# Kernel optimization log

Measured on AMD Instinct MI355X. Metric: run time of the kernel, lower is better.

## Reference

```python
import jax, jax.numpy as jnp
import numpy as np
import math

N_EMBD = 64
HEAD_SIZE = 64
B, T = 16, 2048


def setup_inputs() -> dict:
    key = jax.random.key(0)
    k1, k2, k3, k4 = jax.random.split(key, 4)
    inputs = jax.random.normal(k1, (B, T, N_EMBD), dtype=jnp.float32)
    # Causal mask: True where attention is NOT allowed (upper triangle),
    # matching masked_fill_(mask, -1e9) with mask = ~tril.
    mask = jnp.triu(jnp.ones((T, T), dtype=bool), k=1)
    # nn.Linear(n_embd, head_size, bias=False) weights, stored as
    # (n_embd, head_size) so projection is inputs @ W (== x @ W_torch.T).
    scale = 1.0 / math.sqrt(N_EMBD)
    Wq = jax.random.uniform(k2, (N_EMBD, HEAD_SIZE), jnp.float32, -scale, scale)
    Wk = jax.random.uniform(k3, (N_EMBD, HEAD_SIZE), jnp.float32, -scale, scale)
    Wv = jax.random.uniform(k4, (N_EMBD, HEAD_SIZE), jnp.float32, -scale, scale)
    return {"inputs": inputs, "mask": mask, "Wq": Wq, "Wk": Wk, "Wv": Wv}


def reference(inputs, mask, Wq, Wk, Wv):
    # inputs: (B, T, n_embd); mask: (T, T) bool broadcast over batch
    q = inputs @ Wq  # (B, T, H)
    k = inputs @ Wk  # (B, T, H)
    v = inputs @ Wv  # (B, T, H)
    inv_sqrt_h = 1.0 / math.sqrt(HEAD_SIZE)
    scores = jnp.einsum('bth,bsh->bts', q, k) * inv_sqrt_h  # (B, T, T)
    scores = jnp.where(mask, jnp.float32(-1e9), scores)
    attention = jax.nn.softmax(scores, axis=-1)
    out = jnp.einsum('bts,bsh->bth', attention, v)  # (B, T, H)
    return out
```

## Files before the change

### kernel.cpp

```cpp
#include <hip/hip_runtime.h>
#include <stdint.h>


typedef __bf16 bf16x8 __attribute__((ext_vector_type(8)));
typedef __bf16 bf16x4 __attribute__((ext_vector_type(4)));
typedef float f32x4 __attribute__((ext_vector_type(4)));

#define QSCALE 0.18033688011112042f
#define MFMA16(a, b, c) __builtin_amdgcn_mfma_f32_16x16x32_bf16((a), (b), (c), 0, 0, 0)

__device__ __forceinline__ unsigned short f2bf(float f) {
  union { float f; unsigned u; } x; x.f = f;
  unsigned r = x.u + 0x7fffu + ((x.u >> 16) & 1u);
  return (unsigned short)(r >> 16);
}

__device__ __forceinline__ int swz(int row, int bytecol) {
  return row * 128 + (bytecol ^ ((row & 7) << 4));
}
__device__ __forceinline__ bf16x8 frag(const unsigned short* base, int row, int kf, int lane) {
  int off = swz(row, kf * 64 + ((lane >> 4) << 4));
  return *(const bf16x8*)((const char*)base + off);
}

__device__ __forceinline__ void gload_lds16(const unsigned short* g, unsigned short* l) {
  __builtin_amdgcn_global_load_lds(
      (const __attribute__((address_space(1))) unsigned int*)g,
      (__attribute__((address_space(3))) unsigned int*)l, 16, 0, 0);
}

__global__ __launch_bounds__(256, 2) void proj_kernel(
    const float* __restrict__ X, const float* __restrict__ Wq,
    const float* __restrict__ Wk, const float* __restrict__ Wv,
    unsigned short* __restrict__ Qg, unsigned short* __restrict__ Kg,
    unsigned short* __restrict__ Vtg) {
  __shared__ __align__(16) unsigned short Xs[64 * 64];
  __shared__ __align__(16) unsigned short Ws[3 * 64 * 64];
  const int tid = threadIdx.x, lane = tid & 63, w = tid >> 6;
  const int ln = lane & 15, g = lane >> 4;
  const long grow0 = (long)blockIdx.x * 64;
  const int b = (int)(grow0 >> 11);
  const int tin0 = (int)(grow0 & 2047);

  {
    const int r = tid >> 2, c = tid & 3;
    const float* src = X + (grow0 + r) * 64 + c * 16;
    float4 f0 = *(const float4*)src;
    float4 f1 = *(const float4*)(src + 4);
    float4 f2 = *(const float4*)(src + 8);
    float4 f3 = *(const float4*)(src + 12);
    uint4 d0, d1;
    d0.x = f2bf(f0.x) | ((unsigned)f2bf(f0.y) << 16);
    d0.y = f2bf(f0.z) | ((unsigned)f2bf(f0.w) << 16);
    d0.z = f2bf(f1.x) | ((unsigned)f2bf(f1.y) << 16);
    d0.w = f2bf(f1.z) | ((unsigned)f2bf(f1.w) << 16);
    d1.x = f2bf(f2.x) | ((unsigned)f2bf(f2.y) << 16);
    d1.y = f2bf(f2.z) | ((unsigned)f2bf(f2.w) << 16);
    d1.z = f2bf(f3.x) | ((unsigned)f2bf(f3.y) << 16);
    d1.w = f2bf(f3.z) | ((unsigned)f2bf(f3.w) << 16);
    *(uint4*)((char*)Xs + swz(r, c * 32)) = d0;
    *(uint4*)((char*)Xs + swz(r, c * 32 + 16)) = d1;
  }
  for (int c = tid; c < 3 * 4096; c += 256) {
    const int mat = c >> 12, rr = c & 4095;
    const int e = rr >> 6, hh = rr & 63;
    const float* wsrc = (mat == 0) ? Wq : (mat == 1) ? Wk : Wv;
    *(unsigned short*)((char*)(Ws + mat * 4096) + swz(hh, e * 2)) = f2bf(wsrc[rr]);
  }
  __syncthreads();

  const f32x4 zero = {0.f, 0.f, 0.f, 0.f};
#pragma unroll
  for (int i = 0; i < 3; ++i) {
    const int task = w * 3 + i;
    const int mat = task >> 2, s = task & 3;
    const unsigned short* wbase = Ws + mat * 4096;
    if (mat < 2) {
      bf16x8 a0 = frag(Xs, s * 16 + ln, 0, lane);
      bf16x8 a1 = frag(Xs, s * 16 + ln, 1, lane);
      unsigned short* dst = mat ? Kg : Qg;
#pragma unroll
      for (int nt = 0; nt < 4; ++nt) {
        bf16x8 b0 = frag(wbase, nt * 16 + ln, 0, lane);
        bf16x8 b1 = frag(wbase, nt * 16 + ln, 1, lane);
        f32x4 acc = MFMA16(a0, b0, zero);
        acc = MFMA16(a1, b1, acc);
        long row0 = grow0 + s * 16 + g * 4;
        int col = nt * 16 + ln;
#pragma unroll
        for (int k = 0; k < 4; ++k) {
          float v = acc[k];
          if (mat == 0) v *= QSCALE;
          dst[(row0 + k) * 64 + col] = f2bf(v);
        }
      }
    } else {
      bf16x8 a0 = frag(wbase, s * 16 + ln, 0, lane);
      bf16x8 a1 = frag(wbase, s * 16 + ln, 1, lane);
#pragma unroll
      for (int nt = 0; nt < 4; ++nt) {
        bf16x8 b0 = frag(Xs, nt * 16 + ln, 0, lane);
        bf16x8 b1 = frag(Xs, nt * 16 + ln, 1, lane);
        f32x4 acc = MFMA16(a0, b0, zero);
        acc = MFMA16(a1, b1, acc);
        int t = tin0 + nt * 16 + ln;
        int h0 = s * 16 + g * 4;
#pragma unroll
        for (int k = 0; k < 4; ++k)
          Vtg[((long)(b * 64 + h0 + k)) * 2048 + t] = f2bf(acc[k]);
      }
    }
  }
}

__global__ __launch_bounds__(256, 4) void attn8_kernel(
    const unsigned short* __restrict__ Qg, const unsigned short* __restrict__ Kg,
    const unsigned short* __restrict__ Vtg, float* __restrict__ Og) {
  __shared__ __align__(16) unsigned char smem[35840];

  const int bid = blockIdx.x;
  const int slot = bid >> 3;
  const int b = ((bid & 7) << 1) + (slot & 1);
  const int j = slot >> 1;
  const int qt = (j & 1) ? (j >> 1) : 63 - (j >> 1);
  const int q0 = qt * 32;
  const int ns = (q0 + 95) >> 6;

  const int tid = threadIdx.x;
  const int lane = tid & 63, w = tid >> 6;
  const int g = lane >> 4, ln = lane & 15;
  const int h = w & 1, qh = w >> 1;

  const unsigned short* qrow = Qg + ((long)b * 2048 + q0 + qh * 16 + ln) * 64;
  const bf16x8 qb0 = *(const bf16x8*)(qrow + g * 8);
  const bf16x8 qb1 = *(const bf16x8*)(qrow + 32 + g * 8);

  const unsigned short* kbase = Kg + (long)b * 2048 * 64;
  const unsigned short* vbase = Vtg + (long)b * 64 * 2048;

  const int sw32 = (w & 1) * 32;
  const int cxor = ((lane & 7) ^ ((lane >> 3) & 7)) * 8;
  const int klane = (lane >> 3) * 64 + cxor;
  const int vlane = (lane >> 3) * 2048 + cxor;

  const f32x4 zero = {0.f, 0.f, 0.f, 0.f};
  f32x4 o[4];
#pragma unroll
  for (int nt = 0; nt < 4; ++nt) o[nt] = zero;
  float den = 0.f;

  if (w < 2) {
#pragma unroll
    for (int i = 0; i < 4; ++i)
      gload_lds16(kbase + (long)(sw32 + i * 8) * 64 + klane,
                  (unsigned short*)smem + (sw32 + i * 8) * 64);
  } else {
#pragma unroll
    for (int i = 0; i < 4; ++i)
      gload_lds16(vbase + (long)(sw32 + i * 8) * 2048 + vlane,
                  (unsigned short*)(smem + 8192) + (sw32 + i * 8) * 64);
  }
  __syncthreads();

  int cur = 0;
  for (int t = 0; t < ns; ++t) {
    const int kv0 = t * 64;
    if (t + 1 < ns) {
      const int kvn = kv0 + 64;
      unsigned short* dstK = (unsigned short*)(smem + (cur ^ 1) * 16384);
      unsigned short* dstV = (unsigned short*)(smem + (cur ^ 1) * 16384 + 8192);
      if (w < 2) {
#pragma unroll
        for (int i = 0; i < 4; ++i)
          gload_lds16(kbase + (long)(kvn + sw32 + i * 8) * 64 + klane,
                      dstK + (sw32 + i * 8) * 64);
      } else {
#pragma unroll
        for (int i = 0; i < 4; ++i)
          gload_lds16(vbase + (long)(sw32 + i * 8) * 2048 + kvn + vlane,
                      dstV + (sw32 + i * 8) * 64);
      }
    }

    const unsigned short* Kb = (const unsigned short*)(smem + cur * 16384);
    const unsigned char*  Vb = smem + cur * 16384 + 8192;

    bf16x8 ka00 = frag(Kb, h * 32 + ln,      0, lane);
    bf16x8 ka01 = frag(Kb, h * 32 + ln,      1, lane);
    bf16x8 ka10 = frag(Kb, h * 32 + 16 + ln, 0, lane);
    bf16x8 ka11 = frag(Kb, h * 32 + 16 + ln, 1, lane);

    bf16x8 vb[4];
#pragma unroll
    for (int nt = 0; nt < 4; ++nt) {
      int row = nt * 16 + ln;
      bf16x4 lo = *(const bf16x4*)(Vb + swz(row, h * 64 + g * 8));
      bf16x4 hi = *(const bf16x4*)(Vb + swz(row, h * 64 + 32 + g * 8));
      vb[nt] = __builtin_shufflevector(lo, hi, 0, 1, 2, 3, 4, 5, 6, 7);
    }

    __builtin_amdgcn_s_setprio(1);
    f32x4 st0 = MFMA16(ka00, qb0, zero);  st0 = MFMA16(ka01, qb1, st0);
    f32x4 st1 = MFMA16(ka10, qb0, zero);  st1 = MFMA16(ka11, qb1, st1);
    __builtin_amdgcn_s_setprio(0);

    if (t == ns - 1) {
      const int qg = q0 + qh * 16 + ln;
      const int kvb = kv0 + h * 32 + g * 4;
#pragma unroll
      for (int i = 0; i < 4; ++i) {
        if (kvb + i > qg)      st0[i] = -1e30f;
        if (kvb + 16 + i > qg) st1[i] = -1e30f;
      }
    }

    bf16x8 pa;
#pragma unroll
    for (int i = 0; i < 4; ++i) {
      float p0 = exp2f(st0[i]);
      float p1 = exp2f(st1[i]);
      den += p0 + p1;
      pa[i] = (__bf16)p0;
      pa[4 + i] = (__bf16)p1;
    }

    __builtin_amdgcn_s_setprio(1);
#pragma unroll
    for (int nt = 0; nt < 4; ++nt)
      o[nt] = MFMA16(pa, vb[nt], o[nt]);
    __builtin_amdgcn_s_setprio(0);

    __syncthreads();
    cur ^= 1;
  }

  den += __shfl_xor(den, 16);
  den += __shfl_xor(den, 32);

  float* Olds = (float*)smem;
  float* Dlds = (float*)(smem + 34816);
#pragma unroll
  for (int nt = 0; nt < 4; ++nt)
#pragma unroll
    for (int i = 0; i < 4; ++i)
      Olds[(w * 16 + g * 4 + i) * 68 + nt * 16 + ln] = o[nt][i];
  if (lane < 16) Dlds[w * 16 + ln] = den;
  __syncthreads();

  const int q = tid >> 3;
  const int qhx = q >> 4, r = q & 15;
  const int d0 = (tid & 7) * 8;
  float dd = Dlds[(qhx * 2) * 16 + r] + Dlds[(qhx * 2 + 1) * 16 + r];
  float inv = 1.0f / dd;
  float acc[8];
#pragma unroll
  for (int e = 0; e < 8; ++e)
    acc[e] = (Olds[((qhx * 2) * 16 + r) * 68 + d0 + e] +
              Olds[((qhx * 2 + 1) * 16 + r) * 68 + d0 + e]) * inv;
  float* outp = Og + ((long)b * 2048 + q0 + q) * 64 + d0;
  *(float4*)outp = make_float4(acc[0], acc[1], acc[2], acc[3]);
  *(float4*)(outp + 4) = make_float4(acc[4], acc[5], acc[6], acc[7]);
}

extern "C" void kernel_launch(void* const* d_in, const int* in_sizes, int n_in,
                              void* d_out, int out_size, void* d_ws, size_t ws_size,
                              hipStream_t stream) {
  const float* X  = (const float*)d_in[0];
  const float* Wq = (const float*)d_in[2];
  const float* Wk = (const float*)d_in[3];
  const float* Wv = (const float*)d_in[4];

  unsigned short* Qg  = (unsigned short*)d_ws;
  unsigned short* Kg  = Qg + 2097152;
  unsigned short* Vtg = Kg + 2097152;

  proj_kernel<<<512, 256, 0, stream>>>(X, Wq, Wk, Wv, Qg, Kg, Vtg);
  attn8_kernel<<<1024, 256, 0, stream>>>(Qg, Kg, Vtg, (float*)d_out);
}
```

Measured before the change: 47.60 us.

## Triple-buffer K/V staging with one barrier per iteration

```diff
diff --git a/kernel.cpp b/kernel.cpp
--- a/kernel.cpp
+++ b/kernel.cpp
@@ -113,10 +113,10 @@
   }
 }
 
-__global__ __launch_bounds__(256, 4) void attn8_kernel(
+__global__ __launch_bounds__(256, 3) void attn9_kernel(
     const unsigned short* __restrict__ Qg, const unsigned short* __restrict__ Kg,
     const unsigned short* __restrict__ Vtg, float* __restrict__ Og) {
-  __shared__ __align__(16) unsigned char smem[35840];
+  __shared__ __align__(16) unsigned char smem[49152];
 
   const int bid = blockIdx.x;
   const int slot = bid >> 3;
@@ -142,6 +142,7 @@
   const int cxor = ((lane & 7) ^ ((lane >> 3) & 7)) * 8;
   const int klane = (lane >> 3) * 64 + cxor;
   const int vlane = (lane >> 3) * 2048 + cxor;
+  const bool stagesK = (w < 2);
 
   const f32x4 zero = {0.f, 0.f, 0.f, 0.f};
   f32x4 o[4];
@@ -149,41 +150,41 @@
   for (int nt = 0; nt < 4; ++nt) o[nt] = zero;
   float den = 0.f;
 
-  if (w < 2) {
-#pragma unroll
-    for (int i = 0; i < 4; ++i)
-      gload_lds16(kbase + (long)(sw32 + i * 8) * 64 + klane,
-                  (unsigned short*)smem + (sw32 + i * 8) * 64);
-  } else {
-#pragma unroll
-    for (int i = 0; i < 4; ++i)
-      gload_lds16(vbase + (long)(sw32 + i * 8) * 2048 + vlane,
-                  (unsigned short*)(smem + 8192) + (sw32 + i * 8) * 64);
-  }
-  __syncthreads();
+  auto stage = [&](int t, int bi) {
+    unsigned short* dstK = (unsigned short*)(smem + bi * 16384);
+    unsigned short* dstV = dstK + 4096;
+    const int kv0s = t * 64;
+    if (stagesK) {
+#pragma unroll
+      for (int i = 0; i < 4; ++i)
+        gload_lds16(kbase + (long)(kv0s + sw32 + i * 8) * 64 + klane,
+                    dstK + (sw32 + i * 8) * 64);
+    } else {
+#pragma unroll
+      for (int i = 0; i < 4; ++i)
+        gload_lds16(vbase + (long)(sw32 + i * 8) * 2048 + kv0s + vlane,
+                    dstV + (sw32 + i * 8) * 64);
+    }
+  };
+
+  stage(0, 0);
+  if (ns > 1) stage(1, 1);
 
   int cur = 0;
   for (int t = 0; t < ns; ++t) {
-    const int kv0 = t * 64;
-    if (t + 1 < ns) {
-      const int kvn = kv0 + 64;
-      unsigned short* dstK = (unsigned short*)(smem + (cur ^ 1) * 16384);
-      unsigned short* dstV = (unsigned short*)(smem + (cur ^ 1) * 16384 + 8192);
-      if (w < 2) {
-#pragma unroll
-        for (int i = 0; i < 4; ++i)
-          gload_lds16(kbase + (long)(kvn + sw32 + i * 8) * 64 + klane,
-                      dstK + (sw32 + i * 8) * 64);
-      } else {
-#pragma unroll
-        for (int i = 0; i < 4; ++i)
-          gload_lds16(vbase + (long)(sw32 + i * 8) * 2048 + kvn + vlane,
-                      dstV + (sw32 + i * 8) * 64);
-      }
+    if (t == ns - 1) asm volatile("s_waitcnt vmcnt(0)" ::: "memory");
+    else             asm volatile("s_waitcnt vmcnt(4)" ::: "memory");
+    __builtin_amdgcn_s_barrier();
+    __builtin_amdgcn_sched_barrier(0);
+
+    if (t + 2 < ns) {
+      int nxt = cur + 2; if (nxt >= 3) nxt -= 3;
+      stage(t + 2, nxt);
     }
 
     const unsigned short* Kb = (const unsigned short*)(smem + cur * 16384);
     const unsigned char*  Vb = smem + cur * 16384 + 8192;
+    const int kv0 = t * 64;
 
     bf16x8 ka00 = frag(Kb, h * 32 + ln,      0, lane);
     bf16x8 ka01 = frag(Kb, h * 32 + ln,      1, lane);
@@ -230,12 +231,13 @@
       o[nt] = MFMA16(pa, vb[nt], o[nt]);
     __builtin_amdgcn_s_setprio(0);
 
-    __syncthreads();
-    cur ^= 1;
+    ++cur; if (cur >= 3) cur -= 3;
   }
 
   den += __shfl_xor(den, 16);
   den += __shfl_xor(den, 32);
+
+  __syncthreads();
 
   float* Olds = (float*)smem;
   float* Dlds = (float*)(smem + 34816);
@@ -275,5 +277,5 @@
   unsigned short* Vtg = Kg + 2097152;
 
   proj_kernel<<<512, 256, 0, stream>>>(X, Wq, Wk, Wv, Qg, Kg, Vtg);
-  attn8_kernel<<<1024, 256, 0, stream>>>(Qg, Kg, Vtg, (float*)d_out);
-}
+  attn9_kernel<<<1024, 256, 0, stream>>>(Qg, Kg, Vtg, (float*)d_out);
+}
```

Result: slower. 53.67 us (+12.8%).

## Enlarge attention query tile to 64 with per-wave KV split and triple-buffered K

Applied to the files above, without the earlier changes.

```diff
diff --git a/kernel.cpp b/kernel.cpp
--- a/kernel.cpp
+++ b/kernel.cpp
@@ -113,153 +113,195 @@
   }
 }
 
-__global__ __launch_bounds__(256, 4) void attn8_kernel(
+__global__ __launch_bounds__(256, 2) void attn10_kernel(
     const unsigned short* __restrict__ Qg, const unsigned short* __restrict__ Kg,
     const unsigned short* __restrict__ Vtg, float* __restrict__ Og) {
-  __shared__ __align__(16) unsigned char smem[35840];
+  __shared__ __align__(16) unsigned char smem[49152];
 
   const int bid = blockIdx.x;
-  const int slot = bid >> 3;
-  const int b = ((bid & 7) << 1) + (slot & 1);
-  const int j = slot >> 1;
-  const int qt = (j & 1) ? (j >> 1) : 63 - (j >> 1);
-  const int q0 = qt * 32;
-  const int ns = (q0 + 95) >> 6;
+  const int xcd = bid & 7, idx = bid >> 3;
+  const int b = (xcd << 1) + (idx & 1);
+  const int m = idx >> 1;
+  const int qt = (idx & 1) ? (31 - m) : m;
+  const int q0 = qt * 64;
+  const int ns = (q0 + 191) >> 7;
 
   const int tid = threadIdx.x;
   const int lane = tid & 63, w = tid >> 6;
   const int g = lane >> 4, ln = lane & 15;
-  const int h = w & 1, qh = w >> 1;
-
-  const unsigned short* qrow = Qg + ((long)b * 2048 + q0 + qh * 16 + ln) * 64;
-  const bf16x8 qb0 = *(const bf16x8*)(qrow + g * 8);
-  const bf16x8 qb1 = *(const bf16x8*)(qrow + 32 + g * 8);
+
+  const unsigned short* qrow = Qg + ((long)b * 2048 + q0) * 64;
+  bf16x8 qb[4][2];
+#pragma unroll
+  for (int nq = 0; nq < 4; ++nq)
+#pragma unroll
+    for (int kf = 0; kf < 2; ++kf)
+      qb[nq][kf] = *(const bf16x8*)(qrow + (nq * 16 + ln) * 64 + kf * 32 + g * 8);
 
   const unsigned short* kbase = Kg + (long)b * 2048 * 64;
   const unsigned short* vbase = Vtg + (long)b * 64 * 2048;
 
-  const int sw32 = (w & 1) * 32;
-  const int cxor = ((lane & 7) ^ ((lane >> 3) & 7)) * 8;
-  const int klane = (lane >> 3) * 64 + cxor;
-  const int vlane = (lane >> 3) * 2048 + cxor;
+  const int klane = ((lane >> 3) << 6) + (((lane & 7) ^ ((lane >> 3) & 7)) << 3);
+  unsigned short* kslice = (unsigned short*)(smem + w * 4096);
 
   const f32x4 zero = {0.f, 0.f, 0.f, 0.f};
-  f32x4 o[4];
-#pragma unroll
-  for (int nt = 0; nt < 4; ++nt) o[nt] = zero;
-  float den = 0.f;
-
-  if (w < 2) {
+  f32x4 o[4][4];
+#pragma unroll
+  for (int nq = 0; nq < 4; ++nq)
+#pragma unroll
+    for (int nt = 0; nt < 4; ++nt) o[nq][nt] = zero;
+  float den[4] = {0.f, 0.f, 0.f, 0.f};
+
+  {
+    const unsigned short* kg0 = kbase + (long)(w * 32) * 64 + klane;
 #pragma unroll
     for (int i = 0; i < 4; ++i)
-      gload_lds16(kbase + (long)(sw32 + i * 8) * 64 + klane,
-                  (unsigned short*)smem + (sw32 + i * 8) * 64);
-  } else {
-#pragma unroll
-    for (int i = 0; i < 4; ++i)
-      gload_lds16(vbase + (long)(sw32 + i * 8) * 2048 + vlane,
-                  (unsigned short*)(smem + 8192) + (sw32 + i * 8) * 64);
-  }
-  __syncthreads();
+      gload_lds16(kg0 + i * 512, kslice + i * 512);
+    if (ns > 1) {
+      const unsigned short* kg1 = kbase + (long)(128 + w * 32) * 64 + klane;
+#pragma unroll
+      for (int i = 0; i < 4; ++i)
+        gload_lds16(kg1 + i * 512, (unsigned short*)((char*)kslice + 16384) + i * 512);
+    }
+  }
 
   int cur = 0;
   for (int t = 0; t < ns; ++t) {
-    const int kv0 = t * 64;
-    if (t + 1 < ns) {
-      const int kvn = kv0 + 64;
-      unsigned short* dstK = (unsigned short*)(smem + (cur ^ 1) * 16384);
-      unsigned short* dstV = (unsigned short*)(smem + (cur ^ 1) * 16384 + 8192);
-      if (w < 2) {
-#pragma unroll
-        for (int i = 0; i < 4; ++i)
-          gload_lds16(kbase + (long)(kvn + sw32 + i * 8) * 64 + klane,
-                      dstK + (sw32 + i * 8) * 64);
-      } else {
-#pragma unroll
-        for (int i = 0; i < 4; ++i)
-          gload_lds16(vbase + (long)(sw32 + i * 8) * 2048 + kvn + vlane,
-                      dstV + (sw32 + i * 8) * 64);
+    const int kv0w = t * 128 + w * 32;
+
+    const unsigned short* vr = vbase + (long)ln * 2048 + kv0w + g * 4;
+    bf16x4 vl0 = *(const bf16x4*)vr;
+    bf16x4 vh0 = *(const bf16x4*)(vr + 16);
+    bf16x4 vl1 = *(const bf16x4*)(vr + 16 * 2048);
+    bf16x4 vh1 = *(const bf16x4*)(vr + 16 * 2048 + 16);
+    bf16x4 vl2 = *(const bf16x4*)(vr + 32 * 2048);
+    bf16x4 vh2 = *(const bf16x4*)(vr + 32 * 2048 + 16);
+    bf16x4 vl3 = *(const bf16x4*)(vr + 48 * 2048);
+    bf16x4 vh3 = *(const bf16x4*)(vr + 48 * 2048 + 16);
+
+    if (t + 2 < ns) {
+      int nb = cur + 2; if (nb >= 3) nb -= 3;
+      const unsigned short* kg = kbase + (long)((t + 2) * 128 + w * 32) * 64 + klane;
+      unsigned short* dst = (unsigned short*)((char*)kslice + nb * 16384);
+#pragma unroll
+      for (int i = 0; i < 4; ++i)
+        gload_lds16(kg + i * 512, dst + i * 512);
+    }
+
+    if (t + 2 < ns)      asm volatile("s_waitcnt vmcnt(16)" ::: "memory");
+    else if (t + 1 < ns) asm volatile("s_waitcnt vmcnt(12)" ::: "memory");
+    else                 asm volatile("s_waitcnt vmcnt(8)"  ::: "memory");
+    __builtin_amdgcn_sched_barrier(0);
+
+    const unsigned short* Kb = (const unsigned short*)((char*)kslice + cur * 16384);
+
+    bf16x8 ka00 = frag(Kb, ln, 0, lane);
+    bf16x8 ka01 = frag(Kb, ln, 1, lane);
+    bf16x8 ka10 = frag(Kb, 16 + ln, 0, lane);
+    bf16x8 ka11 = frag(Kb, 16 + ln, 1, lane);
+
+    f32x4 st[2][4];
+    __builtin_amdgcn_s_setprio(1);
+#pragma unroll
+    for (int nq = 0; nq < 4; ++nq) {
+      f32x4 a = MFMA16(ka00, qb[nq][0], zero);
+      st[0][nq] = MFMA16(ka01, qb[nq][1], a);
+      f32x4 c = MFMA16(ka10, qb[nq][0], zero);
+      st[1][nq] = MFMA16(ka11, qb[nq][1], c);
+    }
+    __builtin_amdgcn_s_setprio(0);
+
+    if (t == ns - 1) {
+#pragma unroll
+      for (int s = 0; s < 2; ++s)
+#pragma unroll
+        for (int nq = 0; nq < 4; ++nq) {
+          const int qg = q0 + nq * 16 + ln;
+          const int kvb = kv0w + s * 16 + g * 4;
+#pragma unroll
+          for (int i = 0; i < 4; ++i)
+            if (kvb + i > qg) st[s][nq][i] = -1e30f;
+        }
+    }
+
+    bf16x8 pa[4];
+#pragma unroll
+    for (int nq = 0; nq < 4; ++nq)
+#pragma unroll
+      for (int i = 0; i < 4; ++i) {
+        float p0 = exp2f(st[0][nq][i]);
+        float p1 = exp2f(st[1][nq][i]);
+        den[nq] += p0 + p1;
+        pa[nq][i] = (__bf16)p0;
+        pa[nq][4 + i] = (__bf16)p1;
       }
-    }
-
-    const unsigned short* Kb = (const unsigned short*)(smem + cur * 16384);
-    const unsigned char*  Vb = smem + cur * 16384 + 8192;
-
-    bf16x8 ka00 = frag(Kb, h * 32 + ln,      0, lane);
-    bf16x8 ka01 = frag(Kb, h * 32 + ln,      1, lane);
-    bf16x8 ka10 = frag(Kb, h * 32 + 16 + ln, 0, lane);
-    bf16x8 ka11 = frag(Kb, h * 32 + 16 + ln, 1, lane);
-
-    bf16x8 vb[4];
-#pragma unroll
-    for (int nt = 0; nt < 4; ++nt) {
-      int row = nt * 16 + ln;
-      bf16x4 lo = *(const bf16x4*)(Vb + swz(row, h * 64 + g * 8));
-      bf16x4 hi = *(const bf16x4*)(Vb + swz(row, h * 64 + 32 + g * 8));
-      vb[nt] = __builtin_shufflevector(lo, hi, 0, 1, 2, 3, 4, 5, 6, 7);
-    }
 
     __builtin_amdgcn_s_setprio(1);
-    f32x4 st0 = MFMA16(ka00, qb0, zero);  st0 = MFMA16(ka01, qb1, st0);
-    f32x4 st1 = MFMA16(ka10, qb0, zero);  st1 = MFMA16(ka11, qb1, st1);
+    {
+      bf16x8 vb = __builtin_shufflevector(vl0, vh0, 0, 1, 2, 3, 4, 5, 6, 7);
+#pragma unroll
+      for (int nq = 0; nq < 4; ++nq) o[nq][0] = MFMA16(pa[nq], vb, o[nq][0]);
+      vb = __builtin_shufflevector(vl1, vh1, 0, 1, 2, 3, 4, 5, 6, 7);
+#pragma unroll
+      for (int nq = 0; nq < 4; ++nq) o[nq][1] = MFMA16(pa[nq], vb, o[nq][1]);
+      vb = __builtin_shufflevector(vl2, vh2, 0, 1, 2, 3, 4, 5, 6, 7);
+#pragma unroll
+      for (int nq = 0; nq < 4; ++nq) o[nq][2] = MFMA16(pa[nq], vb, o[nq][2]);
+      vb = __builtin_shufflevector(vl3, vh3, 0, 1, 2, 3, 4, 5, 6, 7);
+#pragma unroll
+      for (int nq = 0; nq < 4; ++nq) o[nq][3] = MFMA16(pa[nq], vb, o[nq][3]);
+    }
     __builtin_amdgcn_s_setprio(0);
 
-    if (t == ns - 1) {
-      const int qg = q0 + qh * 16 + ln;
-      const int kvb = kv0 + h * 32 + g * 4;
-#pragma unroll
-      for (int i = 0; i < 4; ++i) {
-        if (kvb + i > qg)      st0[i] = -1e30f;
-        if (kvb + 16 + i > qg) st1[i] = -1e30f;
-      }
-    }
-
-    bf16x8 pa;
-#pragma unroll
-    for (int i = 0; i < 4; ++i) {
-      float p0 = exp2f(st0[i]);
-      float p1 = exp2f(st1[i]);
-      den += p0 + p1;
-      pa[i] = (__bf16)p0;
-      pa[4 + i] = (__bf16)p1;
-    }
-
-    __builtin_amdgcn_s_setprio(1);
-#pragma unroll
-    for (int nt = 0; nt < 4; ++nt)
-      o[nt] = MFMA16(pa, vb[nt], o[nt]);
-    __builtin_amdgcn_s_setprio(0);
-
-    __syncthreads();
-    cur ^= 1;
-  }
-
-  den += __shfl_xor(den, 16);
-  den += __shfl_xor(den, 32);
-
+    ++cur; if (cur >= 3) cur -= 3;
+  }
+
+#pragma unroll
+  for (int nq = 0; nq < 4; ++nq) {
+    den[nq] += __shfl_xor(den[nq], 16);
+    den[nq] += __shfl_xor(den[nq], 32);
+  }
+
+  __syncthreads();
   float* Olds = (float*)smem;
   float* Dlds = (float*)(smem + 34816);
 #pragma unroll
-  for (int nt = 0; nt < 4; ++nt)
-#pragma unroll
-    for (int i = 0; i < 4; ++i)
-      Olds[(w * 16 + g * 4 + i) * 68 + nt * 16 + ln] = o[nt][i];
-  if (lane < 16) Dlds[w * 16 + ln] = den;
+  for (int nq = 0; nq < 4; ++nq)
+    if (lane < 16) Dlds[w * 64 + nq * 16 + ln] = den[nq];
+  if (w < 2) {
+#pragma unroll
+    for (int nq = 0; nq < 4; ++nq)
+#pragma unroll
+      for (int nt = 0; nt < 4; ++nt)
+#pragma unroll
+        for (int i = 0; i < 4; ++i)
+          Olds[(w * 4352) + (nq * 16 + g * 4 + i) * 68 + nt * 16 + ln] = o[nq][nt][i];
+  }
   __syncthreads();
-
-  const int q = tid >> 3;
-  const int qhx = q >> 4, r = q & 15;
-  const int d0 = (tid & 7) * 8;
-  float dd = Dlds[(qhx * 2) * 16 + r] + Dlds[(qhx * 2 + 1) * 16 + r];
+  if (w >= 2) {
+#pragma unroll
+    for (int nq = 0; nq < 4; ++nq)
+#pragma unroll
+      for (int nt = 0; nt < 4; ++nt)
+#pragma unroll
+        for (int i = 0; i < 4; ++i)
+          Olds[((w - 2) * 4352) + (nq * 16 + g * 4 + i) * 68 + nt * 16 + ln] += o[nq][nt][i];
+  }
+  __syncthreads();
+
+  const int q = tid >> 2;
+  const int d0 = (tid & 3) * 16;
+  float dd = Dlds[q] + Dlds[64 + q] + Dlds[128 + q] + Dlds[192 + q];
   float inv = 1.0f / dd;
-  float acc[8];
-#pragma unroll
-  for (int e = 0; e < 8; ++e)
-    acc[e] = (Olds[((qhx * 2) * 16 + r) * 68 + d0 + e] +
-              Olds[((qhx * 2 + 1) * 16 + r) * 68 + d0 + e]) * inv;
+  float acc[16];
+#pragma unroll
+  for (int e = 0; e < 16; ++e)
+    acc[e] = (Olds[q * 68 + d0 + e] + Olds[4352 + q * 68 + d0 + e]) * inv;
   float* outp = Og + ((long)b * 2048 + q0 + q) * 64 + d0;
-  *(float4*)outp = make_float4(acc[0], acc[1], acc[2], acc[3]);
-  *(float4*)(outp + 4) = make_float4(acc[4], acc[5], acc[6], acc[7]);
+#pragma unroll
+  for (int v4 = 0; v4 < 4; ++v4)
+    *(float4*)(outp + v4 * 4) = make_float4(acc[v4 * 4], acc[v4 * 4 + 1],
+                                            acc[v4 * 4 + 2], acc[v4 * 4 + 3]);
 }
 
 extern "C" void kernel_launch(void* const* d_in, const int* in_sizes, int n_in,
@@ -275,5 +317,5 @@
   unsigned short* Vtg = Kg + 2097152;
 
   proj_kernel<<<512, 256, 0, stream>>>(X, Wq, Wk, Wv, Qg, Kg, Vtg);
-  attn8_kernel<<<1024, 256, 0, stream>>>(Qg, Kg, Vtg, (float*)d_out);
-}
+  attn10_kernel<<<512, 256, 0, stream>>>(Qg, Kg, Vtg, (float*)d_out);
+}
```

Result: slower. 53.17 us (+11.7%).
